# Kernel tuning notes

Measured on AMD Instinct MI355X. Metric: run time of the kernel, lower is better.

Reference implementation:

```python
import jax, jax.numpy as jnp
import numpy as np

PAD_BIG = 1e20  # matches F.pad(value=1e20) on y2


def setup_inputs() -> dict:
    key = jax.random.key(0)
    k1, k2, k3 = jax.random.split(key, 3)
    N, C, H, W = 2, 256, 96, 96
    x = jax.random.normal(k1, (N, C, H, W), dtype=jnp.float32)
    y = jax.random.normal(k2, (N, C, H, W), dtype=jnp.float32)
    labels = jax.random.randint(k3, (N, 1, H, W), 0, 124, dtype=jnp.int32)
    return {"x": x, "y": y, "labels": labels, "max_distance": 4, "num_class": 124}


def _window_stack(p, md, h, w):
    # p: padded [n, c, h+2*md, w+2*md] -> [n, c, h, w, k*k]; offset order
    # (di-major, dj-minor) matches F.unfold column ordering.
    k = 2 * md + 1
    return jnp.stack(
        [p[:, :, di:di + h, dj:dj + w] for di in range(k) for dj in range(k)],
        axis=-1,
    )


def reference(x, y, labels, max_distance, num_class):
    # x: query embedding [N,C,H,W]; y: prev-frame embedding [N,C,H,W]
    # labels: prev-frame labels [N,1,H,W] int
    n, c, h, w = x.shape
    md = max_distance
    k = 2 * md + 1
    kk = k * k

    x2 = jnp.sum(x * x, axis=1)  # [n,h,w]
    y2 = jnp.sum(y * y, axis=1, keepdims=True)  # [n,1,h,w]

    pad_sp = [(0, 0), (0, 0), (md, md), (md, md)]
    py = jnp.pad(y, pad_sp)                                   # zeros
    py2 = jnp.pad(y2, pad_sp, constant_values=PAD_BIG)
    plab = jnp.pad(labels.astype(jnp.float32), pad_sp, constant_values=-1.0)

    y_off = _window_stack(py, md, h, w)          # [n,c,h,w,kk]
    y2_off = _window_stack(py2, md, h, w)[:, 0]  # [n,h,w,kk]
    lab_off = _window_stack(plab, md, h, w)[:, 0]  # [n,h,w,kk]

    corr = jnp.einsum('nchw,nchwp->nhwp', x, y_off)  # [n,h,w,kk]
    d = x2[..., None] + y2_off - 2.0 * corr
    d = (jax.nn.sigmoid(d) - 0.5) * 2.0              # in (-1, 1)

    gt_ids = jnp.arange(num_class, dtype=jnp.float32)
    # mask: [n,h,w,kk,num_class]; padded label -1 never matches -> fill 1.0
    mask = lab_off[..., None] == gt_ids
    dists = jnp.min(jnp.where(mask, d[..., None], 1.0), axis=3)  # [n,h,w,nc]
    return jnp.transpose(dists, (0, 3, 1, 2))  # [n,num_class,h,w]
```

## Files before the change

### kernel.cpp

```cpp
#include <hip/hip_runtime.h>
#include <stdint.h>

#define Nn 2
#define Cc 256
#define Hh 96
#define Ww 96
#define HW (Hh * Ww)
#define MD 4
#define NC 124
#define TH 4
#define TWD 8
#define NQ (TH * TWD)
#define SH (TH + 2 * MD)
#define SWD (TWD + 2 * MD)
#define NS (SH * SWD)
#define BLK 256
#define NBW (Ww / TWD)
#define NBH (Hh / TH)
#define NBLK (Nn * NBH * NBW)
#define YROW 64
#define XOFF (NS * YROW)
#define BUFSZ (XOFF + NQ * YROW)
#define TBL (NQ * NC)
#define CQ 32

#define PPX 256
#define NSTR (HW / PPX)
#define PBLK (2 * Nn * 4 * NSTR)

#define TEN_BYTES ((size_t)Nn * CQ * HW * 16)
#define XT_OFF    TEN_BYTES
#define PART_OFF  (TEN_BYTES * 2)

typedef short short8 __attribute__((ext_vector_type(8)));
typedef float f32x4 __attribute__((ext_vector_type(4)));

__device__ __forceinline__ unsigned fmap(float f) {
    unsigned b = __float_as_uint(f);
    return (b & 0x80000000u) ? ~b : (b | 0x80000000u);
}
__device__ __forceinline__ float funmap(unsigned u) {
    unsigned b = (u & 0x80000000u) ? (u & 0x7fffffffu) : ~u;
    return __uint_as_float(b);
}
__device__ __forceinline__ int swz(int row, int slot) {
    return row * YROW + ((slot ^ ((row >> 1) & 3)) << 4);
}

__global__ __launch_bounds__(256) void prep_t(
    const float* __restrict__ x, const float* __restrict__ y,
    uint4* __restrict__ yT, uint4* __restrict__ xT, float* __restrict__ parts)
{
    __shared__ float tile[64 * PPX];
    const int t = threadIdx.x;
    const int bid = blockIdx.x;
    const int strip = bid % NSTR;
    const int rest  = bid / NSTR;
    const int g4  = rest & 3;
    const int n   = (rest >> 2) & 1;
    const int ten = rest >> 3;
    const int pix0 = strip * PPX;
    const float* src = (ten ? x : y) + ((size_t)n * Cc + g4 * 64) * HW + pix0;
    uint4* dstT = (ten ? xT : yT) + (size_t)n * CQ * HW;

    const int wid = t >> 6, lane = t & 63;
#pragma unroll
    for (int k = 0; k < 16; ++k) {
        const int m = wid * 16 + k;
        const float4 v = *(const float4*)(src + (size_t)m * HW + lane * 4);
        *(float4*)&tile[m * PPX + lane * 4] = v;
    }
    __syncthreads();

    float sq = 0.f;
#pragma unroll
    for (int k = 0; k < 8; ++k) {
        float v[8];
#pragma unroll
        for (int j = 0; j < 8; ++j) v[j] = tile[(k * 8 + j) * PPX + t];
        unsigned pk[4];
#pragma unroll
        for (int j = 0; j < 4; ++j) {
            sq = fmaf(v[2*j],   v[2*j],   sq);
            sq = fmaf(v[2*j+1], v[2*j+1], sq);
            pk[j] = (__float_as_uint(v[2*j]) >> 16) |
                    (__float_as_uint(v[2*j+1]) & 0xffff0000u);
        }
        dstT[(size_t)(g4 * 8 + k) * HW + pix0 + t] =
            make_uint4(pk[0], pk[1], pk[2], pk[3]);
    }
    parts[((size_t)(ten * 4 + g4) * Nn + n) * HW + pix0 + t] = sq;
}

__global__ __launch_bounds__(BLK) void propnet_mfma(
    const uint4* __restrict__ yT, const uint4* __restrict__ xT,
    const float* __restrict__ parts, const int* __restrict__ labels,
    float* __restrict__ out)
{
    __shared__ __align__(16) unsigned char sbuf[2][BUFSZ];
    __shared__ float y2s[NS];
    __shared__ float x2s[NQ];
    __shared__ int   labs[NS];
    unsigned* table = (unsigned*)&sbuf[0][0];

    const int t = threadIdx.x;

    const int orig = blockIdx.x;
    const int lin  = (orig & 7) * (NBLK / 8) + (orig >> 3);
    const int n    = lin / (NBH * NBW);
    const int rem  = lin - n * (NBH * NBW);
    const int h0   = (rem / NBW) * TH;
    const int w0   = (rem % NBW) * TWD;

    const float* ypart = parts;
    const float* xpart = parts + (size_t)4 * Nn * HW;

    if (t < NS) {
        const int sr = t >> 4, sc = t & 15;
        const int gh = h0 - MD + sr, gw = w0 - MD + sc;
        const bool ok = (gh >= 0) && (gh < Hh) && (gw >= 0) && (gw < Ww);
        labs[t] = ok ? labels[(size_t)n * HW + gh * Ww + gw] : -1;
        float s = 0.f;
        if (ok) {
            const size_t idx = (size_t)n * HW + gh * Ww + gw;
#pragma unroll
            for (int g = 0; g < 4; ++g) s += ypart[(size_t)g * Nn * HW + idx];
        }
        y2s[t] = s;
    }
    if (t < NQ) {
        const size_t idx = (size_t)n * HW + (size_t)(h0 + (t >> 3)) * Ww + (w0 + (t & 7));
        float s = 0.f;
#pragma unroll
        for (int g = 0; g < 4; ++g) s += xpart[(size_t)g * Nn * HW + idx];
        x2s[t] = s;
    }

    const int lane = t & 63;
    const int wid  = t >> 6;

    size_t ysrc[3]; int yl[3];
    {
        const int sc4 = lane >> 2;
        const int pos = lane & 3;
        const int cqw = pos ^ ((sc4 >> 1) & 3);
#pragma unroll
        for (int i = 0; i < 3; ++i) {
            const int g  = wid * 3 + i;
            const int gh = min(max(h0 - MD + g, 0), Hh - 1);
            const int gw = min(max(w0 - MD + sc4, 0), Ww - 1);
            ysrc[i] = (size_t)cqw * HW + (size_t)gh * Ww + gw;
            yl[i]   = g * 1024;
        }
    }
    const bool hasx = (wid < 2);
    size_t xsrc = 0; int xl = 0;
    if (hasx) {
        const int q   = wid * 16 + (lane >> 2);
        const int pos = lane & 3;
        const int s   = pos ^ ((q >> 1) & 3);
        xsrc = (size_t)s * HW + (size_t)(h0 + (q >> 3)) * Ww + (w0 + (q & 7));
        xl   = XOFF + wid * 1024;
    }
    const uint4* yTn = yT + (size_t)n * CQ * HW;
    const uint4* xTn = xT + (size_t)n * CQ * HW;
    auto stage = [&](int b, int c) {
        const uint4* yb = yTn + (size_t)(c * 4) * HW;
#pragma unroll
        for (int i = 0; i < 3; ++i)
            __builtin_amdgcn_global_load_lds(
                (const __attribute__((address_space(1))) unsigned int*)(yb + ysrc[i]),
                (__attribute__((address_space(3))) unsigned int*)(sbuf[b] + yl[i]),
                16, 0, 0);
        if (hasx)
            __builtin_amdgcn_global_load_lds(
                (const __attribute__((address_space(1))) unsigned int*)
                    (xTn + (size_t)(c * 4) * HW + xsrc),
                (__attribute__((address_space(3))) unsigned int*)(sbuf[b] + xl),
                16, 0, 0);
    };

    const int l15 = lane & 15;
    const int lg  = lane >> 4;
    int aoff[2], boff[3];
#pragma unroll
    for (int mf = 0; mf < 2; ++mf) aoff[mf] = XOFF + swz(mf * 16 + l15, lg);
#pragma unroll
    for (int nf = 0; nf < 3; ++nf) boff[nf] = swz(wid * 48 + nf * 16 + l15, lg);

    f32x4 acc[2][3];
#pragma unroll
    for (int mf = 0; mf < 2; ++mf)
#pragma unroll
        for (int nf = 0; nf < 3; ++nf)
            acc[mf][nf] = (f32x4){0.f, 0.f, 0.f, 0.f};

    auto compute = [&](const unsigned char* bb) {
        short8 a[2], b[3];
#pragma unroll
        for (int mf = 0; mf < 2; ++mf) a[mf] = *(const short8*)(bb + aoff[mf]);
#pragma unroll
        for (int nf = 0; nf < 3; ++nf) b[nf] = *(const short8*)(bb + boff[nf]);
#pragma unroll
        for (int mf = 0; mf < 2; ++mf)
#pragma unroll
            for (int nf = 0; nf < 3; ++nf)
                acc[mf][nf] = __builtin_amdgcn_mfma_f32_16x16x32_bf16(
                    a[mf], b[nf], acc[mf][nf], 0, 0, 0);
    };

    stage(0, 0);
    __syncthreads();
    for (int c = 0; c < 8; ++c) {
        const int b = c & 1;
        if (c < 7) stage(b ^ 1, c + 1);
        compute(sbuf[b]);
        __syncthreads();
    }

    for (int i = t; i < TBL; i += BLK) table[i] = 0xBF800000u;
    __syncthreads();

#pragma unroll
    for (int mf = 0; mf < 2; ++mf) {
#pragma unroll
        for (int nf = 0; nf < 3; ++nf) {
#pragma unroll
            for (int r = 0; r < 4; ++r) {
                const int q = mf * 16 + lg * 4 + r;
                const int s = wid * 48 + nf * 16 + l15;
                const int qr = q >> 3, qc = q & 7;
                const int sr = s >> 4, sc = s & 15;
                const int di = sr - qr, dj = sc - qc;
                const int lab = labs[s];
                if (di >= 0 && di <= 2 * MD && dj >= 0 && dj <= 2 * MD &&
                    lab >= 0 && lab < NC) {
                    const float d  = x2s[q] + y2s[s] - 2.0f * acc[mf][nf][r];
                    const float sg = 1.0f / (1.0f + __expf(-d));
                    atomicMin(&table[q * NC + lab], fmap(fmaf(2.0f, sg, -1.0f)));
                }
            }
        }
    }
    __syncthreads();

    const size_t ob = (size_t)n * NC * HW;
    for (int i = t; i < TBL; i += BLK) {
        const int g = i >> 5;
        const int q = i & 31;
        const int qr = q >> 3, qc = q & 7;
        out[ob + (size_t)g * HW + (size_t)(h0 + qr) * Ww + (w0 + qc)] =
            funmap(table[q * NC + g]);
    }
}

extern "C" void kernel_launch(void* const* d_in, const int* in_sizes, int n_in,
                              void* d_out, int out_size, void* d_ws, size_t ws_size,
                              hipStream_t stream) {
    const float* x      = (const float*)d_in[0];
    const float* y      = (const float*)d_in[1];
    const int*   labels = (const int*)d_in[2];
    float*       out    = (float*)d_out;
    uint4* yT    = (uint4*)d_ws;
    uint4* xT    = (uint4*)((char*)d_ws + XT_OFF);
    float* parts = (float*)((char*)d_ws + PART_OFF);
    (void)in_sizes; (void)n_in; (void)out_size; (void)ws_size;

    prep_t<<<dim3(PBLK), dim3(256), 0, stream>>>(x, y, yT, xT, parts);
    propnet_mfma<<<dim3(NBLK), dim3(BLK), 0, stream>>>(yT, xT, parts, labels, out);
}
```

Baseline: 32.16 us.

## Stage four channel chunks per phase with vmcnt-gated barriers instead of double buffering

```diff
diff --git a/kernel.cpp b/kernel.cpp
--- a/kernel.cpp
+++ b/kernel.cpp
@@ -21,6 +21,7 @@
 #define YROW 64
 #define XOFF (NS * YROW)
 #define BUFSZ (XOFF + NQ * YROW)
+#define NST 4
 #define TBL (NQ * NC)
 #define CQ 32
 
@@ -92,16 +93,16 @@
     parts[((size_t)(ten * 4 + g4) * Nn + n) * HW + pix0 + t] = sq;
 }
 
-__global__ __launch_bounds__(BLK) void propnet_mfma(
+__global__ __launch_bounds__(BLK, 2) void propnet_mfma(
     const uint4* __restrict__ yT, const uint4* __restrict__ xT,
     const float* __restrict__ parts, const int* __restrict__ labels,
     float* __restrict__ out)
 {
-    __shared__ __align__(16) unsigned char sbuf[2][BUFSZ];
+    __shared__ __align__(16) unsigned char S[NST * BUFSZ];
     __shared__ float y2s[NS];
     __shared__ float x2s[NQ];
     __shared__ int   labs[NS];
-    unsigned* table = (unsigned*)&sbuf[0][0];
+    unsigned* table = (unsigned*)S;
 
     const int t = threadIdx.x;
 
@@ -135,6 +136,7 @@
         for (int g = 0; g < 4; ++g) s += xpart[(size_t)g * Nn * HW + idx];
         x2s[t] = s;
     }
+    asm volatile("s_waitcnt vmcnt(0)" ::: "memory");
 
     const int lane = t & 63;
     const int wid  = t >> 6;
@@ -153,31 +155,36 @@
             yl[i]   = g * 1024;
         }
     }
-    const bool hasx = (wid < 2);
-    size_t xsrc = 0; int xl = 0;
-    if (hasx) {
-        const int q   = wid * 16 + (lane >> 2);
+    size_t xsrc[2]; int xl[2];
+#pragma unroll
+    for (int j = 0; j < 2; ++j) {
+        const int q   = j * 16 + (lane >> 2);
         const int pos = lane & 3;
         const int s   = pos ^ ((q >> 1) & 3);
-        xsrc = (size_t)s * HW + (size_t)(h0 + (q >> 3)) * Ww + (w0 + (q & 7));
-        xl   = XOFF + wid * 1024;
+        xsrc[j] = (size_t)s * HW + (size_t)(h0 + (q >> 3)) * Ww + (w0 + (q & 7));
+        xl[j]   = wid * BUFSZ + XOFF + j * 1024;
     }
     const uint4* yTn = yT + (size_t)n * CQ * HW;
     const uint4* xTn = xT + (size_t)n * CQ * HW;
-    auto stage = [&](int b, int c) {
-        const uint4* yb = yTn + (size_t)(c * 4) * HW;
-#pragma unroll
-        for (int i = 0; i < 3; ++i)
+
+    auto stage_phase = [&](int p) {
+        const size_t xc = (size_t)((p * 4 + wid) * 4) * HW;
+#pragma unroll
+        for (int j = 0; j < 2; ++j)
             __builtin_amdgcn_global_load_lds(
-                (const __attribute__((address_space(1))) unsigned int*)(yb + ysrc[i]),
-                (__attribute__((address_space(3))) unsigned int*)(sbuf[b] + yl[i]),
+                (const __attribute__((address_space(1))) unsigned int*)(xTn + xc + xsrc[j]),
+                (__attribute__((address_space(3))) unsigned int*)(S + xl[j]),
                 16, 0, 0);
-        if (hasx)
-            __builtin_amdgcn_global_load_lds(
-                (const __attribute__((address_space(1))) unsigned int*)
-                    (xTn + (size_t)(c * 4) * HW + xsrc),
-                (__attribute__((address_space(3))) unsigned int*)(sbuf[b] + xl),
-                16, 0, 0);
+#pragma unroll
+        for (int cl = 0; cl < 4; ++cl) {
+            const size_t yc = (size_t)((p * 4 + cl) * 4) * HW;
+#pragma unroll
+            for (int i = 0; i < 3; ++i)
+                __builtin_amdgcn_global_load_lds(
+                    (const __attribute__((address_space(1))) unsigned int*)(yTn + yc + ysrc[i]),
+                    (__attribute__((address_space(3))) unsigned int*)(S + cl * BUFSZ + yl[i]),
+                    16, 0, 0);
+        }
     };
 
     const int l15 = lane & 15;
@@ -209,14 +216,29 @@
                     a[mf], b[nf], acc[mf][nf], 0, 0, 0);
     };
 
-    stage(0, 0);
-    __syncthreads();
-    for (int c = 0; c < 8; ++c) {
-        const int b = c & 1;
-        if (c < 7) stage(b ^ 1, c + 1);
-        compute(sbuf[b]);
-        __syncthreads();
-    }
+#define GATE(N)                                                      \
+    asm volatile("s_waitcnt vmcnt(" #N ")" ::: "memory");            \
+    __builtin_amdgcn_sched_barrier(0);                               \
+    __builtin_amdgcn_s_barrier();                                    \
+    __builtin_amdgcn_sched_barrier(0);
+
+    stage_phase(0);
+    GATE(9); compute(S);
+    GATE(6); compute(S + BUFSZ);
+    GATE(3); compute(S + 2 * BUFSZ);
+    GATE(0); compute(S + 3 * BUFSZ);
+    asm volatile("s_waitcnt lgkmcnt(0)" ::: "memory");
+    __builtin_amdgcn_sched_barrier(0);
+    __builtin_amdgcn_s_barrier();
+    __builtin_amdgcn_sched_barrier(0);
+    stage_phase(1);
+    GATE(9); compute(S);
+    GATE(6); compute(S + BUFSZ);
+    GATE(3); compute(S + 2 * BUFSZ);
+    GATE(0); compute(S + 3 * BUFSZ);
+#undef GATE
+
+    __syncthreads();
 
     for (int i = t; i < TBL; i += BLK) table[i] = 0xBF800000u;
     __syncthreads();
```

Result: slower. 35.78 us (+11.3%).
